# Performance work log

Hardware: AMD Instinct MI355X
Metric: run time of the kernel (lower is better)

The kernel has to match this reference:

```python
import jax, jax.numpy as jnp
import numpy as np

C, W, H = 256, 64, 192
RECORD_LEN = np.array([5, 3, 4, 2, 5, 3, 4, 2], dtype=np.int64)  # sums to 28


def setup_inputs() -> dict:
    key = jax.random.key(0)
    total = int(RECORD_LEN.sum())
    x = jax.random.normal(key, (total, C, W, H), dtype=jnp.float32)
    record_len = jnp.asarray(RECORD_LEN)
    return {"x": x, "record_len": record_len}


def _group_attention(xx):
    # xx: [L, C, W, H] -> per-pixel self-attention over the L agents, d_model = C
    L = xx.shape[0]
    q = xx.reshape(L, C, W * H).transpose(2, 0, 1)          # [N=W*H, L, C]
    score = jnp.einsum('nlc,nmc->nlm', q, q) / jnp.sqrt(jnp.float32(C))
    attn = jax.nn.softmax(score, axis=-1)                    # [N, L, L]
    # original keeps only ego agent (row 0) of the context
    ctx0 = jnp.einsum('nm,nmc->nc', attn[:, 0, :], q)        # [N, C]
    out = ctx0.T.reshape(1, C, W, H)
    attn_maps = attn.transpose(1, 2, 0).reshape(L, L, W, H)
    return out, attn_maps


def reference(x, record_len):
    rl = np.asarray(record_len)  # static ragged lengths
    offsets = np.concatenate([[0], np.cumsum(rl)])
    outs = []
    attn_last = None
    for i in range(len(rl)):  # small fixed number of ragged groups
        xx = x[int(offsets[i]):int(offsets[i + 1])]
        out_i, attn_last = _group_attention(xx)
        outs.append(out_i)
    # matches torch: returns fused ego features per scene + attn of LAST group
    return jnp.concatenate(outs, axis=0), attn_last
```

## Files before the change

### kernel.cpp

```cpp
#include <hip/hip_runtime.h>
#include <math.h>

#define C_DIM 256
#define W_DIM 64
#define H_DIM 192
#define WH (W_DIM * H_DIM)
#define NGROUPS 8
#define NCHUNK 16
#define CCH (C_DIM / NCHUNK)
#define NLOC 32
#define NBLK (WH / NLOC)
#define BLOCK 512

template <int L, bool WRITE_ATTN>
__device__ __forceinline__ void att_body(
    const float* __restrict__ xg,
    float* __restrict__ out,
    float* __restrict__ attn_out,
    float* __restrict__ lds,
    const int n, const int chunk, const int nl)
{
    constexpr int NTRI = L * (L + 1) / 2;
    constexpr int NACC = WRITE_ATTN ? NTRI : L;
    static_assert(NACC <= 5, "LDS sized for <=5 accumulators");

    const int c0 = chunk * CCH;

    float v[L][CCH];
#pragma unroll
    for (int cc = 0; cc < CCH; ++cc)
#pragma unroll
        for (int l = 0; l < L; ++l)
            v[l][cc] = xg[(size_t)(l * C_DIM + c0 + cc) * WH + n];

    float s[NACC];
#pragma unroll
    for (int i = 0; i < NACC; ++i) s[i] = 0.0f;

    if constexpr (WRITE_ATTN) {
#pragma unroll
        for (int cc = 0; cc < CCH; ++cc) {
            int idx = 0;
#pragma unroll
            for (int l = 0; l < L; ++l)
#pragma unroll
                for (int m = l; m < L; ++m)
                    s[idx++] += v[l][cc] * v[m][cc];
        }
    } else {
#pragma unroll
        for (int cc = 0; cc < CCH; ++cc)
#pragma unroll
            for (int m = 0; m < L; ++m)
                s[m] += v[0][cc] * v[m][cc];
    }

#pragma unroll
    for (int i = 0; i < NACC; ++i)
        lds[i * BLOCK + chunk * NLOC + nl] = s[i];
    __syncthreads();

    float sf[NACC];
#pragma unroll
    for (int i = 0; i < NACC; ++i) {
        float a = 0.0f;
#pragma unroll
        for (int ch = 0; ch < NCHUNK; ++ch)
            a += lds[i * BLOCK + ch * NLOC + nl];
        sf[i] = a;
    }

    const float scale = 0.0625f;

    float p0[L];
    float mx = -INFINITY;
#pragma unroll
    for (int m = 0; m < L; ++m) {
        p0[m] = sf[m] * scale;
        mx = fmaxf(mx, p0[m]);
    }
    float sum = 0.0f;
#pragma unroll
    for (int m = 0; m < L; ++m) {
        p0[m] = __expf(p0[m] - mx);
        sum += p0[m];
    }
    const float inv = 1.0f / sum;
#pragma unroll
    for (int m = 0; m < L; ++m) p0[m] *= inv;

    if constexpr (WRITE_ATTN) {
        if (chunk < L) {
            const int r = chunk;
            float row[L];
#pragma unroll
            for (int m = 0; m < L; ++m) {
                const int lo = (r < m) ? r : m;
                const int hi = (r < m) ? m : r;
                const int idx = lo * L - lo * (lo - 1) / 2 + (hi - lo);
                row[m] = sf[idx] * scale;
            }
            float mx2 = -INFINITY;
#pragma unroll
            for (int m = 0; m < L; ++m) mx2 = fmaxf(mx2, row[m]);
            float e[L];
            float sm = 0.0f;
#pragma unroll
            for (int m = 0; m < L; ++m) {
                e[m] = __expf(row[m] - mx2);
                sm += e[m];
            }
            const float iv = 1.0f / sm;
#pragma unroll
            for (int m = 0; m < L; ++m)
                __builtin_nontemporal_store(
                    e[m] * iv, &attn_out[(size_t)(r * L + m) * WH + n]);
        }
    }

#pragma unroll
    for (int cc = 0; cc < CCH; ++cc) {
        float acc = 0.0f;
#pragma unroll
        for (int m = 0; m < L; ++m)
            acc += p0[m] * v[m][cc];
        __builtin_nontemporal_store(acc, &out[(size_t)(c0 + cc) * WH + n]);
    }
}

__global__ __launch_bounds__(BLOCK, 3) void att_fused_kernel(
    const float* __restrict__ x,
    float* __restrict__ out0,
    float* __restrict__ attn)
{
    __shared__ float lds[5 * BLOCK];

    const int b = blockIdx.x;
    const int g = b / NBLK;
    const int bn = b - g * NBLK;
    const int chunk = threadIdx.x >> 5;
    const int nl = threadIdx.x & 31;
    const int n = bn * NLOC + nl;

    const int offs[NGROUPS] = {0, 5, 8, 12, 14, 19, 22, 26};
    const int lens[NGROUPS] = {5, 3, 4, 2, 5, 3, 4, 2};

    const float* xg = x + (size_t)offs[g] * C_DIM * WH;
    float* og = out0 + (size_t)g * C_DIM * WH;

    switch (lens[g]) {
        case 5: att_body<5, false>(xg, og, nullptr, lds, n, chunk, nl); break;
        case 4: att_body<4, false>(xg, og, nullptr, lds, n, chunk, nl); break;
        case 3: att_body<3, false>(xg, og, nullptr, lds, n, chunk, nl); break;
        case 2:
            if (g == NGROUPS - 1)
                att_body<2, true>(xg, og, attn, lds, n, chunk, nl);
            else
                att_body<2, false>(xg, og, nullptr, lds, n, chunk, nl);
            break;
    }
}

extern "C" void kernel_launch(void* const* d_in, const int* in_sizes, int n_in,
                              void* d_out, int out_size, void* d_ws, size_t ws_size,
                              hipStream_t stream) {
    const float* x = (const float*)d_in[0];
    float* out0 = (float*)d_out;
    float* attn = out0 + (size_t)NGROUPS * C_DIM * WH;

    const dim3 grid(NGROUPS * NBLK);
    const dim3 block(BLOCK);
    att_fused_kernel<<<grid, block, 0, stream>>>(x, out0, attn);
}
```

Before: 501.2 us.

## Vectorize pixel loads to float4, shuffle-reduce channel partials, widen block

Each thread now handles 4 adjacent pixels with float4 nontemporal loads and stores, and 2 channels instead of 16. The block is 1024 threads covering 128 channel chunks. Partial dot products are reduced inside each wave with xor shuffles before a smaller LDS cross-wave reduction. The aim is wider memory transactions, fewer registers per thread and less LDS traffic, at the cost of more shuffle work and larger blocks.

```diff
diff --git a/kernel.cpp b/kernel.cpp
--- a/kernel.cpp
+++ b/kernel.cpp
@@ -5,37 +5,56 @@
 #define W_DIM 64
 #define H_DIM 192
 #define WH (W_DIM * H_DIM)
+#define WH4 (WH / 4)
 #define NGROUPS 8
-#define NCHUNK 16
-#define CCH (C_DIM / NCHUNK)
 #define NLOC 32
+#define NQUAD (NLOC / 4)
+#define NCHUNK 128
+#define CCH 2
+#define BLOCK 1024
 #define NBLK (WH / NLOC)
-#define BLOCK 512
+
+typedef float v4 __attribute__((ext_vector_type(4)));
+
+__device__ __forceinline__ v4 v4_max(v4 a, v4 b) {
+    v4 r;
+    r[0] = fmaxf(a[0], b[0]); r[1] = fmaxf(a[1], b[1]);
+    r[2] = fmaxf(a[2], b[2]); r[3] = fmaxf(a[3], b[3]);
+    return r;
+}
+__device__ __forceinline__ v4 v4_exp(v4 a) {
+    v4 r;
+    r[0] = __expf(a[0]); r[1] = __expf(a[1]);
+    r[2] = __expf(a[2]); r[3] = __expf(a[3]);
+    return r;
+}
 
 template <int L, bool WRITE_ATTN>
 __device__ __forceinline__ void att_body(
     const float* __restrict__ xg,
     float* __restrict__ out,
     float* __restrict__ attn_out,
-    float* __restrict__ lds,
-    const int n, const int chunk, const int nl)
+    v4* __restrict__ lds,
+    const int n4, const int chunk, const int quad, const int wave)
 {
     constexpr int NTRI = L * (L + 1) / 2;
     constexpr int NACC = WRITE_ATTN ? NTRI : L;
     static_assert(NACC <= 5, "LDS sized for <=5 accumulators");
 
     const int c0 = chunk * CCH;
-
-    float v[L][CCH];
+    const v4* xg4 = reinterpret_cast<const v4*>(xg);
+
+    v4 v[L][CCH];
 #pragma unroll
     for (int cc = 0; cc < CCH; ++cc)
 #pragma unroll
         for (int l = 0; l < L; ++l)
-            v[l][cc] = xg[(size_t)(l * C_DIM + c0 + cc) * WH + n];
-
-    float s[NACC];
-#pragma unroll
-    for (int i = 0; i < NACC; ++i) s[i] = 0.0f;
+            v[l][cc] = __builtin_nontemporal_load(
+                &xg4[(size_t)(l * C_DIM + c0 + cc) * WH4 + n4]);
+
+    v4 s[NACC];
+#pragma unroll
+    for (int i = 0; i < NACC; ++i) s[i] = (v4)0.0f;
 
     if constexpr (WRITE_ATTN) {
 #pragma unroll
@@ -56,91 +75,111 @@
     }
 
 #pragma unroll
-    for (int i = 0; i < NACC; ++i)
-        lds[i * BLOCK + chunk * NLOC + nl] = s[i];
+    for (int k = 8; k < 64; k <<= 1) {
+#pragma unroll
+        for (int i = 0; i < NACC; ++i) {
+            v4 t;
+#pragma unroll
+            for (int j = 0; j < 4; ++j)
+                t[j] = __shfl_xor(s[i][j], k);
+            s[i] += t;
+        }
+    }
+
+    if ((threadIdx.x & 63) < 8) {
+#pragma unroll
+        for (int i = 0; i < NACC; ++i)
+            lds[(i * 16 + wave) * NQUAD + quad] = s[i];
+    }
     __syncthreads();
 
-    float sf[NACC];
+    v4 sf[NACC];
 #pragma unroll
     for (int i = 0; i < NACC; ++i) {
-        float a = 0.0f;
-#pragma unroll
-        for (int ch = 0; ch < NCHUNK; ++ch)
-            a += lds[i * BLOCK + ch * NLOC + nl];
+        v4 a = lds[(i * 16 + 0) * NQUAD + quad];
+#pragma unroll
+        for (int w = 1; w < 16; ++w)
+            a += lds[(i * 16 + w) * NQUAD + quad];
         sf[i] = a;
     }
 
     const float scale = 0.0625f;
 
-    float p0[L];
-    float mx = -INFINITY;
+    v4 p0[L];
+    v4 mx = (v4)(-INFINITY);
 #pragma unroll
     for (int m = 0; m < L; ++m) {
         p0[m] = sf[m] * scale;
-        mx = fmaxf(mx, p0[m]);
-    }
-    float sum = 0.0f;
+        mx = v4_max(mx, p0[m]);
+    }
+    v4 sum = (v4)0.0f;
 #pragma unroll
     for (int m = 0; m < L; ++m) {
-        p0[m] = __expf(p0[m] - mx);
+        p0[m] = v4_exp(p0[m] - mx);
         sum += p0[m];
     }
-    const float inv = 1.0f / sum;
+    v4 inv;
+#pragma unroll
+    for (int j = 0; j < 4; ++j) inv[j] = 1.0f / sum[j];
 #pragma unroll
     for (int m = 0; m < L; ++m) p0[m] *= inv;
 
     if constexpr (WRITE_ATTN) {
         if (chunk < L) {
             const int r = chunk;
-            float row[L];
+            v4 row[L];
+            v4 mx2 = (v4)(-INFINITY);
 #pragma unroll
             for (int m = 0; m < L; ++m) {
                 const int lo = (r < m) ? r : m;
                 const int hi = (r < m) ? m : r;
                 const int idx = lo * L - lo * (lo - 1) / 2 + (hi - lo);
                 row[m] = sf[idx] * scale;
+                mx2 = v4_max(mx2, row[m]);
             }
-            float mx2 = -INFINITY;
-#pragma unroll
-            for (int m = 0; m < L; ++m) mx2 = fmaxf(mx2, row[m]);
-            float e[L];
-            float sm = 0.0f;
+            v4 sm = (v4)0.0f;
+            v4 e[L];
 #pragma unroll
             for (int m = 0; m < L; ++m) {
-                e[m] = __expf(row[m] - mx2);
+                e[m] = v4_exp(row[m] - mx2);
                 sm += e[m];
             }
-            const float iv = 1.0f / sm;
+            v4 iv;
+#pragma unroll
+            for (int j = 0; j < 4; ++j) iv[j] = 1.0f / sm[j];
+            v4* ao4 = reinterpret_cast<v4*>(attn_out);
 #pragma unroll
             for (int m = 0; m < L; ++m)
                 __builtin_nontemporal_store(
-                    e[m] * iv, &attn_out[(size_t)(r * L + m) * WH + n]);
+                    e[m] * iv, &ao4[(size_t)(r * L + m) * WH4 + n4]);
         }
     }
 
+    v4* out4 = reinterpret_cast<v4*>(out);
 #pragma unroll
     for (int cc = 0; cc < CCH; ++cc) {
-        float acc = 0.0f;
+        v4 acc = (v4)0.0f;
 #pragma unroll
         for (int m = 0; m < L; ++m)
             acc += p0[m] * v[m][cc];
-        __builtin_nontemporal_store(acc, &out[(size_t)(c0 + cc) * WH + n]);
-    }
-}
-
-__global__ __launch_bounds__(BLOCK, 3) void att_fused_kernel(
+        __builtin_nontemporal_store(acc, &out4[(size_t)(c0 + cc) * WH4 + n4]);
+    }
+}
+
+__global__ __launch_bounds__(BLOCK, 4) void att_fused_kernel(
     const float* __restrict__ x,
     float* __restrict__ out0,
     float* __restrict__ attn)
 {
-    __shared__ float lds[5 * BLOCK];
+    __shared__ v4 lds[5 * 16 * NQUAD];
 
     const int b = blockIdx.x;
     const int g = b / NBLK;
     const int bn = b - g * NBLK;
-    const int chunk = threadIdx.x >> 5;
-    const int nl = threadIdx.x & 31;
-    const int n = bn * NLOC + nl;
+    const int chunk = threadIdx.x >> 3;
+    const int quad = threadIdx.x & 7;
+    const int wave = threadIdx.x >> 6;
+    const int n4 = bn * NQUAD + quad;
 
     const int offs[NGROUPS] = {0, 5, 8, 12, 14, 19, 22, 26};
     const int lens[NGROUPS] = {5, 3, 4, 2, 5, 3, 4, 2};
@@ -149,14 +188,14 @@
     float* og = out0 + (size_t)g * C_DIM * WH;
 
     switch (lens[g]) {
-        case 5: att_body<5, false>(xg, og, nullptr, lds, n, chunk, nl); break;
-        case 4: att_body<4, false>(xg, og, nullptr, lds, n, chunk, nl); break;
-        case 3: att_body<3, false>(xg, og, nullptr, lds, n, chunk, nl); break;
+        case 5: att_body<5, false>(xg, og, nullptr, lds, n4, chunk, quad, wave); break;
+        case 4: att_body<4, false>(xg, og, nullptr, lds, n4, chunk, quad, wave); break;
+        case 3: att_body<3, false>(xg, og, nullptr, lds, n4, chunk, quad, wave); break;
         case 2:
             if (g == NGROUPS - 1)
-                att_body<2, true>(xg, og, attn, lds, n, chunk, nl);
+                att_body<2, true>(xg, og, attn, lds, n4, chunk, quad, wave);
             else
-                att_body<2, false>(xg, og, nullptr, lds, n, chunk, nl);
+                att_body<2, false>(xg, og, nullptr, lds, n4, chunk, quad, wave);
             break;
     }
 }
```

Result: no change. 492.6 us (-1.7%).
